# Kernel optimization log

Hardware: AMD Instinct MI355X
Metric: run time of the kernel (lower is better)

## Reference

```python
import jax, jax.numpy as jnp
import numpy as np


def _normalize_adj(adj):
    # GCNConv default: add self-loops (weight 1.0), symmetric normalization
    # A_hat = A + I;  norm = D^{-1/2} A_hat D^{-1/2}
    N = adj.shape[-1]
    a_hat = adj + jnp.eye(N, dtype=adj.dtype)          # [B,N,N]
    deg = a_hat.sum(axis=-1)                            # [B,N]
    d_inv_sqrt = jnp.where(deg > 0, deg ** -0.5, 0.0)   # [B,N]
    return d_inv_sqrt[:, :, None] * a_hat * d_inv_sqrt[:, None, :]


def setup_inputs() -> dict:
    key = jax.random.key(0)
    ks = jax.random.split(key, 4)
    B, N, F, H = 16, 2048, 64, 128
    x = jax.random.normal(ks[0], (B, N, F), dtype=jnp.float32)
    adj = jax.random.uniform(ks[1], (B, N, N), dtype=jnp.float32)
    W1 = jax.random.normal(ks[2], (F, H), dtype=jnp.float32) * (1.0 / np.sqrt(F))
    b1 = jnp.zeros((H,), dtype=jnp.float32)
    W2 = jax.random.normal(ks[3], (H, H), dtype=jnp.float32) * (1.0 / np.sqrt(H))
    b2 = jnp.zeros((H,), dtype=jnp.float32)
    return {"x": x, "adj": adj, "W1": W1, "b1": b1, "W2": W2, "b2": b2}


def reference(x, adj, W1, b1, W2, b2):
    # Batched equivalent of per-sample GCNConv -> relu -> dropout(eval) -> GCNConv -> relu
    norm = _normalize_adj(adj)                              # [B,N,N]
    h = jnp.einsum('bij,bjh->bih', norm, x @ W1) + b1       # GCNConv 1
    h = jax.nn.relu(h)                                      # dropout is identity in eval
    h = jnp.einsum('bij,bjh->bih', norm, h @ W2) + b2       # GCNConv 2
    return jax.nn.relu(h)
```

## Files before the change

kernel.cpp:

```cpp
#include <hip/hip_runtime.h>

typedef float  f32x4 __attribute__((ext_vector_type(4)));
typedef short  s16x8 __attribute__((ext_vector_type(8)));

#define GLB_AS(p) ((const __attribute__((address_space(1))) unsigned int*)(p))
#define LDS_AS(p) ((__attribute__((address_space(3))) unsigned int*)(p))

__device__ __forceinline__ void gl_lds16(const void* g, void* l) {
  __builtin_amdgcn_global_load_lds(GLB_AS(g), LDS_AS(l), 16, 0, 0);
}

__device__ __forceinline__ unsigned short f2bf(float f) {
  union { float f; unsigned u; } v; v.f = f;
  unsigned r = v.u + 0x7fffu + ((v.u >> 16) & 1u);
  return (unsigned short)(r >> 16);
}

__global__ __launch_bounds__(256) void k_prep(
    const float* __restrict__ adj, const float* __restrict__ x,
    const float* __restrict__ W1, const float* __restrict__ W2,
    unsigned short* __restrict__ adjh, unsigned short* __restrict__ xh,
    unsigned short* __restrict__ w1t, unsigned short* __restrict__ w2t,
    float* __restrict__ dinv)
{
  __shared__ float red[4];
  int bid = blockIdx.x, t = threadIdx.x;
  if (bid < 32768) {
    int row = bid & 2047;
    const float4* src = (const float4*)(adj + (size_t)bid * 2048) + t * 2;
    float4 v0 = src[0], v1 = src[1];
    float vals[8] = {v0.x, v0.y, v0.z, v0.w, v1.x, v1.y, v1.z, v1.w};
    int c0 = t * 8;
    float s = 0.f;
    s16x8 ob;
#pragma unroll
    for (int i = 0; i < 8; ++i) {
      float v = vals[i] + ((c0 + i) == row ? 1.0f : 0.0f);
      s += v;
      ob[i] = (short)f2bf(v);
    }
    *(s16x8*)(adjh + (size_t)bid * 2048 + c0) = ob;
#pragma unroll
    for (int off = 32; off > 0; off >>= 1) s += __shfl_down(s, off, 64);
    if ((t & 63) == 0) red[t >> 6] = s;
    __syncthreads();
    if (t == 0) dinv[bid] = rsqrtf(red[0] + red[1] + red[2] + red[3]);
  } else if (bid < 32768 + 1024) {
    size_t base = (size_t)(bid - 32768) * 2048 + (size_t)t * 8;
    float4 v0 = *(const float4*)(x + base);
    float4 v1 = *(const float4*)(x + base + 4);
    float vals[8] = {v0.x, v0.y, v0.z, v0.w, v1.x, v1.y, v1.z, v1.w};
    s16x8 ob;
#pragma unroll
    for (int i = 0; i < 8; ++i) ob[i] = (short)f2bf(vals[i]);
    *(s16x8*)(xh + base) = ob;
  } else if (bid == 33792) {
#pragma unroll 4
    for (int i = 0; i < 32; ++i) {
      int idx = t * 32 + i; int h = idx >> 6, k = idx & 63;
      w1t[h * 64 + k] = f2bf(W1[k * 128 + h]);
    }
  } else {
#pragma unroll 4
    for (int i = 0; i < 64; ++i) {
      int idx = t * 64 + i; int h = idx >> 7, k = idx & 127;
      w2t[h * 128 + k] = f2bf(W2[k * 128 + h]);
    }
  }
}

template<int K>
__global__ __launch_bounds__(256) void k_small(
    const unsigned short* __restrict__ A,
    const unsigned short* __restrict__ Wt,
    const float* __restrict__ dinv,
    unsigned short* __restrict__ Zt)
{
  constexpr int CH = K / 8;
  constexpr int CSH = (CH == 8) ? 3 : 4;
  constexpr int LDSB = (2 * 128 * K * 2 > 33280) ? 2 * 128 * K * 2 : 33280;
  __shared__ __align__(16) char lds[LDSB];
  unsigned short* As = (unsigned short*)lds;
  unsigned short* Bs = As + 128 * K;
  unsigned short* tr = (unsigned short*)lds;

  int t = threadIdx.x;
  int w = t >> 6, lane = t & 63;
  int b = blockIdx.x >> 4, m0 = (blockIdx.x & 15) << 7;
  const unsigned short* Ab = A + ((size_t)b * 2048 + m0) * K;

#pragma unroll
  for (int it = 0; it < CH / 2; ++it) {
    int s = it * 256 + t;
    int row = s >> CSH, c = s & (CH - 1);
    int sc = c ^ (row & 7);
    int dst = (it * 256 + (t & 192)) * 16;
    gl_lds16(Ab + (size_t)row * K + sc * 8, (char*)As + dst);
    gl_lds16(Wt + (size_t)row * K + sc * 8, (char*)Bs + dst);
  }
  __syncthreads();

  int wr = w >> 1, wc = w & 1;
  int g = lane >> 4, r16 = lane & 15;
  f32x4 acc[4][4] = {};
#pragma unroll
  for (int kk = 0; kk < K / 32; ++kk) {
    s16x8 af[4], bfr[4];
#pragma unroll
    for (int m = 0; m < 4; ++m) {
      int row = wr * 64 + m * 16 + r16;
      int sc = (kk * 4 + g) ^ (row & 7);
      af[m] = *(const s16x8*)(As + row * K + sc * 8);
    }
#pragma unroll
    for (int n = 0; n < 4; ++n) {
      int row = wc * 64 + n * 16 + r16;
      int sc = (kk * 4 + g) ^ (row & 7);
      bfr[n] = *(const s16x8*)(Bs + row * K + sc * 8);
    }
#pragma unroll
    for (int m = 0; m < 4; ++m)
#pragma unroll
      for (int n = 0; n < 4; ++n)
        acc[m][n] = __builtin_amdgcn_mfma_f32_16x16x32_bf16(af[m], bfr[n], acc[m][n], 0, 0, 0);
  }
  __syncthreads();

#pragma unroll
  for (int m = 0; m < 4; ++m) {
#pragma unroll
    for (int rr = 0; rr < 4; ++rr) {
      int rloc = wr * 64 + m * 16 + g * 4 + rr;
      float dv = dinv[b * 2048 + m0 + rloc];
#pragma unroll
      for (int n = 0; n < 4; ++n) {
        int col = wc * 64 + n * 16 + r16;
        tr[rloc * 130 + col] = f2bf(acc[m][n][rr] * dv);
      }
    }
  }
  __syncthreads();

  int h = t >> 1, half = t & 1;
  unsigned short* Zrow = Zt + ((size_t)b * 128 + h) * 2048 + m0 + half * 64;
#pragma unroll
  for (int jj = 0; jj < 8; ++jj) {
    s16x8 pk;
#pragma unroll
    for (int i = 0; i < 8; ++i) pk[i] = (short)tr[(half * 64 + jj * 8 + i) * 130 + h];
    *(s16x8*)(Zrow + jj * 8) = pk;
  }
}

template<bool BF16OUT>
__global__ __launch_bounds__(256) void k_big(
    const unsigned short* __restrict__ Ah,
    const unsigned short* __restrict__ Zt,
    const float* __restrict__ dinv,
    const float* __restrict__ bias,
    void* __restrict__ outp)
{
  __shared__ __align__(16) unsigned short As[64 * 64];
  __shared__ __align__(16) unsigned short Bs[128 * 64];
  int t = threadIdx.x;
  int w = t >> 6, lane = t & 63;
  int b = blockIdx.x >> 5, mt = blockIdx.x & 31;
  int m0 = mt << 6;
  const unsigned short* Ab = Ah + (size_t)b * 2048 * 2048 + (size_t)m0 * 2048;
  const unsigned short* Zb = Zt + (size_t)b * 128 * 2048;
  int wr = w >> 1, wc = w & 1;
  int g = lane >> 4, r16 = lane & 15;
  f32x4 acc[2][4] = {};

  for (int kt = 0; kt < 32; ++kt) {
#pragma unroll
    for (int it = 0; it < 2; ++it) {
      int s = it * 256 + t;
      int row = s >> 3, c = s & 7;
      int sc = c ^ (row & 7);
      gl_lds16(Ab + (size_t)row * 2048 + kt * 64 + sc * 8,
               (char*)As + (it * 256 + (t & 192)) * 16);
    }
#pragma unroll
    for (int it = 0; it < 4; ++it) {
      int s = it * 256 + t;
      int row = s >> 3, c = s & 7;
      int sc = c ^ (row & 7);
      gl_lds16(Zb + (size_t)row * 2048 + kt * 64 + sc * 8,
               (char*)Bs + (it * 256 + (t & 192)) * 16);
    }
    __syncthreads();
#pragma unroll
    for (int kk = 0; kk < 2; ++kk) {
      s16x8 af[2], bfr[4];
#pragma unroll
      for (int m = 0; m < 2; ++m) {
        int row = wr * 32 + m * 16 + r16;
        int sc = (kk * 4 + g) ^ (row & 7);
        af[m] = *(const s16x8*)(As + row * 64 + sc * 8);
      }
#pragma unroll
      for (int n = 0; n < 4; ++n) {
        int row = wc * 64 + n * 16 + r16;
        int sc = (kk * 4 + g) ^ (row & 7);
        bfr[n] = *(const s16x8*)(Bs + row * 64 + sc * 8);
      }
#pragma unroll
      for (int m = 0; m < 2; ++m)
#pragma unroll
        for (int n = 0; n < 4; ++n)
          acc[m][n] = __builtin_amdgcn_mfma_f32_16x16x32_bf16(af[m], bfr[n], acc[m][n], 0, 0, 0);
    }
    __syncthreads();
  }

#pragma unroll
  for (int m = 0; m < 2; ++m) {
#pragma unroll
    for (int rr = 0; rr < 4; ++rr) {
      int grow = m0 + wr * 32 + m * 16 + g * 4 + rr;
      float dv = dinv[b * 2048 + grow];
#pragma unroll
      for (int n = 0; n < 4; ++n) {
        int col = wc * 64 + n * 16 + r16;
        float v = fmaxf(acc[m][n][rr] * dv + bias[col], 0.0f);
        size_t off = ((size_t)b * 2048 + grow) * 128 + col;
        if (BF16OUT) ((unsigned short*)outp)[off] = f2bf(v);
        else         ((float*)outp)[off] = v;
      }
    }
  }
}

extern "C" void kernel_launch(void* const* d_in, const int* in_sizes, int n_in,
                              void* d_out, int out_size, void* d_ws, size_t ws_size,
                              hipStream_t stream)
{
  (void)in_sizes; (void)n_in; (void)out_size; (void)ws_size;
  const float* x   = (const float*)d_in[0];
  const float* adj = (const float*)d_in[1];
  const float* W1  = (const float*)d_in[2];
  const float* b1  = (const float*)d_in[3];
  const float* W2  = (const float*)d_in[4];
  const float* b2  = (const float*)d_in[5];

  char* ws = (char*)d_ws;
  unsigned short* adjh = (unsigned short*)(ws);
  unsigned short* xh   = (unsigned short*)(ws + 134217728);
  unsigned short* w1t  = (unsigned short*)(ws + 138412032);
  unsigned short* w2t  = (unsigned short*)(ws + 138428416);
  float*          dinv = (float*)         (ws + 138461184);
  unsigned short* z1t  = (unsigned short*)(ws + 138592256);
  unsigned short* h1   = (unsigned short*)(ws + 146980864);
  unsigned short* z2t  = (unsigned short*)(ws + 155369472);

  k_prep<<<33794, 256, 0, stream>>>(adj, x, W1, W2, adjh, xh, w1t, w2t, dinv);
  k_small<64><<<256, 256, 0, stream>>>(xh, w1t, dinv, z1t);
  k_big<true><<<512, 256, 0, stream>>>(adjh, z1t, dinv, b1, (void*)h1);
  k_small<128><<<256, 256, 0, stream>>>(h1, w2t, dinv, z2t);
  k_big<false><<<512, 256, 0, stream>>>(adjh, z2t, dinv, b2, d_out);
}
```

Measured before the change: 481.1 us.

## Double-buffer LDS in big GEMM and restructure small GEMM to write transposed output directly

The big adjacency GEMM now double-buffers its LDS tiles, so the async global-to-LDS loads for the next K tile are issued while MFMAs run on the current one. The small feature-transform kernel swaps operand roles (W^T times X^T) over 64-node tiles across twice as many blocks. It writes Zt directly from registers instead of transposing through LDS. The risks are doubled LDS use in the big kernel, which may lower occupancy, and narrower, less coalesced stores in the small kernel.

```diff
diff --git a/kernel.cpp b/kernel.cpp
--- a/kernel.cpp
+++ b/kernel.cpp
@@ -71,41 +71,43 @@
 
 template<int K>
 __global__ __launch_bounds__(256) void k_small(
-    const unsigned short* __restrict__ A,
+    const unsigned short* __restrict__ X,
     const unsigned short* __restrict__ Wt,
     const float* __restrict__ dinv,
     unsigned short* __restrict__ Zt)
 {
-  constexpr int CH = K / 8;
+  constexpr int CH  = K / 8;
   constexpr int CSH = (CH == 8) ? 3 : 4;
-  constexpr int LDSB = (2 * 128 * K * 2 > 33280) ? 2 * 128 * K * 2 : 33280;
-  __shared__ __align__(16) char lds[LDSB];
-  unsigned short* As = (unsigned short*)lds;
-  unsigned short* Bs = As + 128 * K;
-  unsigned short* tr = (unsigned short*)lds;
+  __shared__ __align__(16) unsigned short As[128 * K];
+  __shared__ __align__(16) unsigned short Bs[64 * K];
 
   int t = threadIdx.x;
   int w = t >> 6, lane = t & 63;
-  int b = blockIdx.x >> 4, m0 = (blockIdx.x & 15) << 7;
-  const unsigned short* Ab = A + ((size_t)b * 2048 + m0) * K;
+  int b = blockIdx.x >> 5, node0 = (blockIdx.x & 31) << 6;
+  const unsigned short* Xb = X + ((size_t)b * 2048 + node0) * K;
 
 #pragma unroll
   for (int it = 0; it < CH / 2; ++it) {
     int s = it * 256 + t;
     int row = s >> CSH, c = s & (CH - 1);
     int sc = c ^ (row & 7);
-    int dst = (it * 256 + (t & 192)) * 16;
-    gl_lds16(Ab + (size_t)row * K + sc * 8, (char*)As + dst);
-    gl_lds16(Wt + (size_t)row * K + sc * 8, (char*)Bs + dst);
+    gl_lds16(Wt + (size_t)row * K + sc * 8, (char*)As + (it * 256 + (t & 192)) * 16);
+  }
+#pragma unroll
+  for (int it = 0; it < CH / 4; ++it) {
+    int s = it * 256 + t;
+    int row = s >> CSH, c = s & (CH - 1);
+    int sc = c ^ (row & 7);
+    gl_lds16(Xb + (size_t)row * K + sc * 8, (char*)Bs + (it * 256 + (t & 192)) * 16);
   }
   __syncthreads();
 
   int wr = w >> 1, wc = w & 1;
   int g = lane >> 4, r16 = lane & 15;
-  f32x4 acc[4][4] = {};
+  f32x4 acc[4][2] = {};
 #pragma unroll
   for (int kk = 0; kk < K / 32; ++kk) {
-    s16x8 af[4], bfr[4];
+    s16x8 af[4], bfr[2];
 #pragma unroll
     for (int m = 0; m < 4; ++m) {
       int row = wr * 64 + m * 16 + r16;
@@ -113,42 +115,33 @@
       af[m] = *(const s16x8*)(As + row * K + sc * 8);
     }
 #pragma unroll
-    for (int n = 0; n < 4; ++n) {
-      int row = wc * 64 + n * 16 + r16;
+    for (int n = 0; n < 2; ++n) {
+      int row = wc * 32 + n * 16 + r16;
       int sc = (kk * 4 + g) ^ (row & 7);
       bfr[n] = *(const s16x8*)(Bs + row * K + sc * 8);
     }
 #pragma unroll
     for (int m = 0; m < 4; ++m)
 #pragma unroll
-      for (int n = 0; n < 4; ++n)
+      for (int n = 0; n < 2; ++n)
         acc[m][n] = __builtin_amdgcn_mfma_f32_16x16x32_bf16(af[m], bfr[n], acc[m][n], 0, 0, 0);
   }
-  __syncthreads();
-
+
+  float dv[2];
+#pragma unroll
+  for (int n = 0; n < 2; ++n)
+    dv[n] = dinv[b * 2048 + node0 + wc * 32 + n * 16 + r16];
 #pragma unroll
   for (int m = 0; m < 4; ++m) {
 #pragma unroll
     for (int rr = 0; rr < 4; ++rr) {
-      int rloc = wr * 64 + m * 16 + g * 4 + rr;
-      float dv = dinv[b * 2048 + m0 + rloc];
-#pragma unroll
-      for (int n = 0; n < 4; ++n) {
-        int col = wc * 64 + n * 16 + r16;
-        tr[rloc * 130 + col] = f2bf(acc[m][n][rr] * dv);
-      }
-    }
-  }
-  __syncthreads();
-
-  int h = t >> 1, half = t & 1;
-  unsigned short* Zrow = Zt + ((size_t)b * 128 + h) * 2048 + m0 + half * 64;
-#pragma unroll
-  for (int jj = 0; jj < 8; ++jj) {
-    s16x8 pk;
-#pragma unroll
-    for (int i = 0; i < 8; ++i) pk[i] = (short)tr[(half * 64 + jj * 8 + i) * 130 + h];
-    *(s16x8*)(Zrow + jj * 8) = pk;
+      int h = wr * 64 + m * 16 + g * 4 + rr;
+#pragma unroll
+      for (int n = 0; n < 2; ++n) {
+        int node = node0 + wc * 32 + n * 16 + r16;
+        Zt[((size_t)b * 128 + h) * 2048 + node] = f2bf(acc[m][n][rr] * dv[n]);
+      }
+    }
   }
 }
 
@@ -160,8 +153,8 @@
     const float* __restrict__ bias,
     void* __restrict__ outp)
 {
-  __shared__ __align__(16) unsigned short As[64 * 64];
-  __shared__ __align__(16) unsigned short Bs[128 * 64];
+  __shared__ __align__(16) unsigned short As[2][64 * 64];
+  __shared__ __align__(16) unsigned short Bs[2][128 * 64];
   int t = threadIdx.x;
   int w = t >> 6, lane = t & 63;
   int b = blockIdx.x >> 5, mt = blockIdx.x & 31;
@@ -172,14 +165,14 @@
   int g = lane >> 4, r16 = lane & 15;
   f32x4 acc[2][4] = {};
 
-  for (int kt = 0; kt < 32; ++kt) {
+  auto stage = [&](int kt, int bi) {
 #pragma unroll
     for (int it = 0; it < 2; ++it) {
       int s = it * 256 + t;
       int row = s >> 3, c = s & 7;
       int sc = c ^ (row & 7);
       gl_lds16(Ab + (size_t)row * 2048 + kt * 64 + sc * 8,
-               (char*)As + (it * 256 + (t & 192)) * 16);
+               (char*)As[bi] + (it * 256 + (t & 192)) * 16);
     }
 #pragma unroll
     for (int it = 0; it < 4; ++it) {
@@ -187,9 +180,16 @@
       int row = s >> 3, c = s & 7;
       int sc = c ^ (row & 7);
       gl_lds16(Zb + (size_t)row * 2048 + kt * 64 + sc * 8,
-               (char*)Bs + (it * 256 + (t & 192)) * 16);
-    }
-    __syncthreads();
+               (char*)Bs[bi] + (it * 256 + (t & 192)) * 16);
+    }
+  };
+
+  stage(0, 0);
+  __syncthreads();
+
+  for (int kt = 0; kt < 32; ++kt) {
+    int cur = kt & 1;
+    if (kt < 31) stage(kt + 1, cur ^ 1);
 #pragma unroll
     for (int kk = 0; kk < 2; ++kk) {
       s16x8 af[2], bfr[4];
@@ -197,13 +197,13 @@
       for (int m = 0; m < 2; ++m) {
         int row = wr * 32 + m * 16 + r16;
         int sc = (kk * 4 + g) ^ (row & 7);
-        af[m] = *(const s16x8*)(As + row * 64 + sc * 8);
+        af[m] = *(const s16x8*)(As[cur] + row * 64 + sc * 8);
       }
 #pragma unroll
       for (int n = 0; n < 4; ++n) {
         int row = wc * 64 + n * 16 + r16;
         int sc = (kk * 4 + g) ^ (row & 7);
-        bfr[n] = *(const s16x8*)(Bs + row * 64 + sc * 8);
+        bfr[n] = *(const s16x8*)(Bs[cur] + row * 64 + sc * 8);
       }
 #pragma unroll
       for (int m = 0; m < 2; ++m)
@@ -255,8 +255,8 @@
   unsigned short* z2t  = (unsigned short*)(ws + 155369472);
 
   k_prep<<<33794, 256, 0, stream>>>(adj, x, W1, W2, adjh, xh, w1t, w2t, dinv);
-  k_small<64><<<256, 256, 0, stream>>>(xh, w1t, dinv, z1t);
+  k_small<64><<<512, 256, 0, stream>>>(xh, w1t, dinv, z1t);
   k_big<true><<<512, 256, 0, stream>>>(adjh, z1t, dinv, b1, (void*)h1);
-  k_small<128><<<256, 256, 0, stream>>>(h1, w2t, dinv, z2t);
+  k_small<128><<<512, 256, 0, stream>>>(h1, w2t, dinv, z2t);
   k_big<false><<<512, 256, 0, stream>>>(adjh, z2t, dinv, b2, d_out);
 }
```

New measurement: 481.4 us. About the same (+0.1%).
